# Optimization experiments

Hardware: AMD Instinct MI355X
Metric: run time of the kernel (lower is better)

## Reference

```python
import jax, jax.numpy as jnp
import numpy as np
from jax import lax

GAMMA_FLOW = 0.001
GAMMA_MASK = 0.0005
INTERP_RATIOS = (0.5,)


def setup_inputs() -> dict:
    key = jax.random.key(0)
    k1, k2, k3 = jax.random.split(key, 3)
    N, H, W, Ce = 8, 512, 512, 32
    frames = jax.random.uniform(k1, (N, H, W, 6), dtype=jnp.float32)
    encoded = jax.random.normal(k2, (N, H, W, Ce), dtype=jnp.float32)
    # small init so tanh is not saturated, like a trained conv head
    conv_w = jax.random.normal(k3, (3, 3, Ce, 3), dtype=jnp.float32) * 0.05
    conv_b = jnp.zeros((3,), dtype=jnp.float32)
    return {"frames": frames, "encoded": encoded, "conv_w": conv_w, "conv_b": conv_b}


def _total_variation(x):
    # matches tf.image.total_variation summed over the batch
    return (jnp.sum(jnp.abs(x[:, 1:] - x[:, :-1])) +
            jnp.sum(jnp.abs(x[:, :, 1:] - x[:, :, :-1])))


def _bilinear_interp(image, new_hh, new_ww):
    # image: [N,H,W,C]; new_hh/new_ww: [N,H,W] normalized coords in [-1,1]
    N, H, W, C = image.shape
    hh = (new_hh + 1.0) * (H - 1) / 2.0
    ww = (new_ww + 1.0) * (W - 1) / 2.0
    h0 = jnp.floor(hh).astype(jnp.int32)
    w0 = jnp.floor(ww).astype(jnp.int32)
    h1 = jnp.clip(h0 + 1, 0, H - 1)
    w1 = jnp.clip(w0 + 1, 0, W - 1)
    h0 = jnp.clip(h0, 0, H - 1)
    w0 = jnp.clip(w0, 0, W - 1)
    img_flat = image.reshape(N, H * W, C)

    def gather(h, w):
        idx = (h * W + w).reshape(N, H * W, 1)
        return jnp.take_along_axis(img_flat, idx, axis=1).reshape(N, H, W, C)

    ru = gather(h0, w0)
    rd = gather(h1, w0)
    lu = gather(h0, w1)
    ld = gather(h1, w1)
    h1f = h1.astype(hh.dtype)
    w1f = w1.astype(ww.dtype)
    w_ru = ((h1f - hh) * (w1f - ww))[..., None]
    w_rd = ((1.0 - (h1f - hh)) * (w1f - ww))[..., None]
    w_lu = ((h1f - hh) * (1.0 - (w1f - ww)))[..., None]
    w_ld = ((1.0 - (h1f - hh)) * (1.0 - (w1f - ww)))[..., None]
    return w_ru * ru + w_rd * rd + w_lu * lu + w_ld * ld


def reference(frames, encoded, conv_w, conv_b):
    frame0 = frames[..., 0:3]
    frame1 = frames[..., 3:6]
    N, H, W, _ = frame0.shape
    # 3x3 SAME conv + tanh (the layer's float32 conv head)
    net = jnp.tanh(
        lax.conv_general_dilated(encoded, conv_w, (1, 1), 'SAME',
                                 dimension_numbers=('NHWC', 'HWIO', 'NHWC'))
        + conv_b)
    flow = net[..., 0:2]

    hh = jnp.broadcast_to(jnp.linspace(-1.0, 1.0, H)[None, :, None], (N, H, W))
    ww = jnp.broadcast_to(jnp.linspace(-1.0, 1.0, W)[None, None, :], (N, H, W))

    total_pixels = float(N * H * W * 3)
    tv_loss = GAMMA_FLOW * _total_variation(flow) / total_pixels

    output_frames = []
    for i, alpha in enumerate(INTERP_RATIOS):
        mask = net[..., i + 2:i + 3]
        tv_loss = tv_loss + GAMMA_MASK * _total_variation(mask) / total_pixels
        coor_h_0 = hh + flow[..., 0] * alpha
        coor_w_0 = ww + flow[..., 1] * alpha
        coor_h_1 = hh - flow[..., 0] * (1.0 - alpha)
        coor_w_1 = ww - flow[..., 1] * (1.0 - alpha)
        out0 = _bilinear_interp(frame0, coor_h_0, coor_w_0)
        out1 = _bilinear_interp(frame1, coor_h_1, coor_w_1)
        m = 0.5 * (1.0 + mask)
        output_frames.append(m * out0 + (1.0 - m) * out1)
    stacked = jnp.concatenate(output_frames, axis=-1)
    return stacked, flow, tv_loss
```

## Files before the change

kernel.cpp:

```cpp
#include <hip/hip_runtime.h>
#include <hip/hip_fp16.h>
#include <math.h>

#define HH 512
#define WW 512
#define NIMG 8
#define NPIX (NIMG * HH * WW)
#define GAMMA_FLOW 0.001f
#define GAMMA_MASK 0.0005f
#define INV_TOTAL (1.0f / (float)(NPIX * 3))

#define CVT_BLOCKS  (NPIX / 256)
#define CONV_BLOCKS (NPIX / 128)
#define FAT_BLOCKS  (CVT_BLOCKS + CONV_BLOCKS)

__device__ __forceinline__ float tanh_fast(float x)
{
    float e = __expf(2.0f * x);
    return 1.0f - 2.0f / (e + 1.0f);
}

__device__ __forceinline__ void fma12(float acc[3], const float wf[12],
                                      float4 x)
{
    float xv[4] = {x.x, x.y, x.z, x.w};
#pragma unroll
    for (int k = 0; k < 4; ++k) {
        acc[0] = fmaf(xv[k], wf[k * 3 + 0], acc[0]);
        acc[1] = fmaf(xv[k], wf[k * 3 + 1], acc[1]);
        acc[2] = fmaf(xv[k], wf[k * 3 + 2], acc[2]);
    }
}

__global__ __launch_bounds__(256, 4) void fat_kernel(
    const float* __restrict__ enc, const float* __restrict__ cw,
    const float* __restrict__ cb, const float* __restrict__ frames,
    float* __restrict__ flow, float* __restrict__ mask,
    __half* __restrict__ f0h, __half* __restrict__ f1h,
    float* __restrict__ tv_out)
{
    int bid = blockIdx.x;

    if (bid % 3 == 0) {
        int ci = bid / 3;
        int t  = ci * 256 + threadIdx.x;
        if (t == 0) tv_out[0] = 0.0f;
        const float2* fp = reinterpret_cast<const float2*>(frames + (size_t)t * 6);
        float2 v0 = fp[0], v1 = fp[1], v2 = fp[2];
        __half2 a = __floats2half2_rn(v0.x, v0.y);
        __half2 b = __floats2half2_rn(v1.x, 0.0f);
        __half2 c = __floats2half2_rn(v1.y, v2.x);
        __half2 d = __floats2half2_rn(v2.y, 0.0f);
        __half2* p0 = reinterpret_cast<__half2*>(f0h) + (size_t)t * 2;
        __half2* p1 = reinterpret_cast<__half2*>(f1h) + (size_t)t * 2;
        p0[0] = a; p0[1] = b;
        p1[0] = c; p1[1] = d;
        return;
    }

    int ci  = bid - (bid + 2) / 3;
    int wb  = (ci & 7) * (CONV_BLOCKS / 8) + (ci >> 3);
    int px0 = wb * 128;
    int n = px0 >> 18;
    int h = (px0 >> 9) & (HH - 1);

    int tid  = threadIdx.x;
    int wv   = tid >> 6;
    int lane = tid & 63;
    int pg   = lane >> 3;
    int c4   = lane & 7;

    int wbase = (px0 & (WW - 1)) + wv * 32;
    int pxb   = wbase + pg * 4;

    const float4* cwB = reinterpret_cast<const float4*>(cw) + c4 * 3;
    const float* imgbase = enc + ((size_t)n * HH) * (WW * 32);

    float acc[4][3];
#pragma unroll
    for (int p = 0; p < 4; ++p)
        acc[p][0] = acc[p][1] = acc[p][2] = 0.0f;

    bool edge = (wbase == 0) || (wbase == WW - 32);

#pragma unroll
    for (int kh = 0; kh < 3; ++kh) {
        int hr = h + kh - 1;
        if ((unsigned)hr >= (unsigned)HH) continue;
        const float* rowp = imgbase + (size_t)hr * (WW * 32);

        float4 win[6];
        if (!edge) {
            const float* pB = rowp + (pxb - 1) * 32 + c4 * 4;
#pragma unroll
            for (int j = 0; j < 6; ++j)
                win[j] = *reinterpret_cast<const float4*>(pB + j * 32);
        } else {
#pragma unroll
            for (int j = 0; j < 6; ++j) {
                int col = pxb + j - 1;
                win[j] = make_float4(0.f, 0.f, 0.f, 0.f);
                if ((unsigned)col < (unsigned)WW)
                    win[j] = *reinterpret_cast<const float4*>(
                                 rowp + (size_t)col * 32 + c4 * 4);
            }
        }

#pragma unroll
        for (int kw = 0; kw < 3; ++kw) {
            int t = kh * 3 + kw;
            float wf[12];
            *reinterpret_cast<float4*>(&wf[0]) = cwB[t * 24 + 0];
            *reinterpret_cast<float4*>(&wf[4]) = cwB[t * 24 + 1];
            *reinterpret_cast<float4*>(&wf[8]) = cwB[t * 24 + 2];
#pragma unroll
            for (int p = 0; p < 4; ++p)
                fma12(acc[p], wf, win[p + kw]);
        }
    }

    float b0 = cb[0], b1 = cb[1], b2 = cb[2];
    size_t rowidx = ((size_t)n * HH + h) * WW;

#pragma unroll
    for (int p = 0; p < 4; ++p) {
#pragma unroll
        for (int off = 1; off < 8; off <<= 1) {
            acc[p][0] += __shfl_xor(acc[p][0], off);
            acc[p][1] += __shfl_xor(acc[p][1], off);
            acc[p][2] += __shfl_xor(acc[p][2], off);
        }
    }
    if (c4 == 0) {
#pragma unroll
        for (int p = 0; p < 4; ++p) {
            size_t idx = rowidx + (size_t)(pxb + p);
            *reinterpret_cast<float2*>(flow + idx * 2) =
                make_float2(tanh_fast(acc[p][0] + b0),
                            tanh_fast(acc[p][1] + b1));
            mask[idx] = tanh_fast(acc[p][2] + b2);
        }
    }
}

__device__ __forceinline__ void bilerp_h(const __half* __restrict__ img,
                                         float ch, float cwv, float out[3])
{
    float hp = (ch + 1.0f) * 255.5f;
    float wp = (cwv + 1.0f) * 255.5f;
    int h0 = (int)floorf(hp);
    int w0 = (int)floorf(wp);
    int h1  = min(max(h0 + 1, 0), HH - 1);
    int w1  = min(max(w0 + 1, 0), WW - 1);
    int h0c = min(max(h0, 0), HH - 1);
    int w0c = min(max(w0, 0), WW - 1);
    float wh = (float)h1 - hp;
    float wv = (float)w1 - wp;
    float w_ru = wh * wv;
    float w_rd = (1.0f - wh) * wv;
    float w_lu = wh * (1.0f - wv);
    float w_ld = (1.0f - wh) * (1.0f - wv);

    int q = min(w0c, WW - 2);
    bool Ahi = (w0c != q);
    bool Bhi = (w1 == q + 1);
    float4 U = *reinterpret_cast<const float4*>(img + (size_t)(((h0c << 9) + q) << 2));
    float4 D = *reinterpret_cast<const float4*>(img + (size_t)(((h1  << 9) + q) << 2));
    float ru_ab = Ahi ? U.z : U.x, ru_c = Ahi ? U.w : U.y;
    float rd_ab = Ahi ? D.z : D.x, rd_c = Ahi ? D.w : D.y;
    float lu_ab = Bhi ? U.z : U.x, lu_c = Bhi ? U.w : U.y;
    float ld_ab = Bhi ? D.z : D.x, ld_c = Bhi ? D.w : D.y;

    float2 ruA = __half22float2(*reinterpret_cast<__half2*>(&ru_ab));
    float2 rdA = __half22float2(*reinterpret_cast<__half2*>(&rd_ab));
    float2 luA = __half22float2(*reinterpret_cast<__half2*>(&lu_ab));
    float2 ldA = __half22float2(*reinterpret_cast<__half2*>(&ld_ab));
    float ruZ = __half2float(reinterpret_cast<__half2*>(&ru_c)->x);
    float rdZ = __half2float(reinterpret_cast<__half2*>(&rd_c)->x);
    float luZ = __half2float(reinterpret_cast<__half2*>(&lu_c)->x);
    float ldZ = __half2float(reinterpret_cast<__half2*>(&ld_c)->x);

    out[0] = w_ru * ruA.x + w_rd * rdA.x + w_lu * luA.x + w_ld * ldA.x;
    out[1] = w_ru * ruA.y + w_rd * rdA.y + w_lu * luA.y + w_ld * ldA.y;
    out[2] = w_ru * ruZ   + w_rd * rdZ   + w_lu * luZ   + w_ld * ldZ;
}

__global__ __launch_bounds__(256, 4) void interp_tv_kernel(
    const __half* __restrict__ f0h, const __half* __restrict__ f1h,
    const float* __restrict__ flow, const float* __restrict__ mask,
    float* __restrict__ stacked, float* __restrict__ tv_out)
{
    int bid = blockIdx.x;
    int wb  = (bid & 7) * (NPIX / 2048 / 8) + (bid >> 3);
    int idx0 = wb * 2048 + (int)threadIdx.x * 8;
    int w0 = idx0 & (WW - 1);
    int h  = (idx0 >> 9) & (HH - 1);
    int n  = idx0 >> 18;

    float4 fl[4];
#pragma unroll
    for (int j = 0; j < 4; ++j)
        fl[j] = *reinterpret_cast<const float4*>(flow + (size_t)idx0 * 2 + j * 4);
    float4 mkA = *reinterpret_cast<const float4*>(mask + idx0);
    float4 mkB = *reinterpret_cast<const float4*>(mask + idx0 + 4);
    const float* flp = reinterpret_cast<const float*>(fl);
    float mkp[8] = {mkA.x, mkA.y, mkA.z, mkA.w, mkB.x, mkB.y, mkB.z, mkB.w};

    float hhv = -1.0f + (float)h * (2.0f / 511.0f);

    const __half* i0 = f0h + (size_t)n * (HH * WW * 4);
    const __half* i1 = f1h + (size_t)n * (HH * WW * 4);

    float res[24];
#pragma unroll
    for (int p = 0; p < 8; ++p) {
        float wvx = -1.0f + (float)(w0 + p) * (2.0f / 511.0f);
        float fx = flp[p * 2], fy = flp[p * 2 + 1];
        float o0[3], o1[3];
        bilerp_h(i0, hhv + fx * 0.5f, wvx + fy * 0.5f, o0);
        bilerp_h(i1, hhv - fx * 0.5f, wvx - fy * 0.5f, o1);
        float m = 0.5f * (1.0f + mkp[p]), om = 1.0f - m;
#pragma unroll
        for (int c = 0; c < 3; ++c)
            res[p * 3 + c] = m * o0[c] + om * o1[c];
    }
    float4* sp = reinterpret_cast<float4*>(stacked + (size_t)idx0 * 3);
#pragma unroll
    for (int j = 0; j < 6; ++j)
        sp[j] = make_float4(res[j * 4], res[j * 4 + 1],
                            res[j * 4 + 2], res[j * 4 + 3]);

    float tvf = 0.0f, tvm = 0.0f;
#pragma unroll
    for (int p = 0; p < 7; ++p) {
        tvf += fabsf(flp[p * 2 + 2] - flp[p * 2])
             + fabsf(flp[p * 2 + 3] - flp[p * 2 + 1]);
        tvm += fabsf(mkp[p + 1] - mkp[p]);
    }
    if (w0 < WW - 8) {
        float2 flr = *reinterpret_cast<const float2*>(flow + (size_t)(idx0 + 8) * 2);
        float  mkr = mask[idx0 + 8];
        tvf += fabsf(flr.x - flp[14]) + fabsf(flr.y - flp[15]);
        tvm += fabsf(mkr - mkp[7]);
    }
    if (h < HH - 1) {
#pragma unroll
        for (int j = 0; j < 4; ++j) {
            float4 fd = *reinterpret_cast<const float4*>(
                            flow + (size_t)(idx0 + WW) * 2 + j * 4);
            tvf += fabsf(fd.x - flp[j * 4 + 0]) + fabsf(fd.y - flp[j * 4 + 1])
                 + fabsf(fd.z - flp[j * 4 + 2]) + fabsf(fd.w - flp[j * 4 + 3]);
        }
        float4 mdA = *reinterpret_cast<const float4*>(mask + idx0 + WW);
        float4 mdB = *reinterpret_cast<const float4*>(mask + idx0 + WW + 4);
        tvm += fabsf(mdA.x - mkp[0]) + fabsf(mdA.y - mkp[1])
             + fabsf(mdA.z - mkp[2]) + fabsf(mdA.w - mkp[3])
             + fabsf(mdB.x - mkp[4]) + fabsf(mdB.y - mkp[5])
             + fabsf(mdB.z - mkp[6]) + fabsf(mdB.w - mkp[7]);
    }
    float tv = GAMMA_FLOW * tvf + GAMMA_MASK * tvm;
#pragma unroll
    for (int off = 32; off > 0; off >>= 1) tv += __shfl_xor(tv, off);
    if ((threadIdx.x & 63) == 0) atomicAdd(tv_out, tv * INV_TOTAL);
}

extern "C" void kernel_launch(void* const* d_in, const int* in_sizes, int n_in,
                              void* d_out, int out_size, void* d_ws, size_t ws_size,
                              hipStream_t stream)
{
    const float* frames  = (const float*)d_in[0];
    const float* encoded = (const float*)d_in[1];
    const float* conv_w  = (const float*)d_in[2];
    const float* conv_b  = (const float*)d_in[3];

    float* out     = (float*)d_out;
    float* stacked = out;
    float* flow    = out + (size_t)NPIX * 3;
    float* tv      = out + (size_t)NPIX * 5;

    const size_t frame_bytes = (size_t)NPIX * 4 * sizeof(__half);
    __half* f0h = (__half*)d_ws;
    __half* f1h = (__half*)((char*)d_ws + frame_bytes);
    float*  mask = (float*)((char*)d_ws + 2 * frame_bytes);

    fat_kernel<<<FAT_BLOCKS, 256, 0, stream>>>(
        encoded, conv_w, conv_b, frames, flow, mask, f0h, f1h, tv);
    interp_tv_kernel<<<NPIX / 2048, 256, 0, stream>>>(
        f0h, f1h, flow, mask, stacked, tv);
}
```

Baseline: 223.6 us.

## Split conv: half in fused cvt kernel, half in 8-pixel-per-thread conv kernel

The fused kernel now computes the conv for only the first half of the pixels, interleaved one-to-one with the frame-conversion blocks. A new conv8_kernel handles the second half, with each thread computing 8 output pixels from a 10-column sliding window. This is meant to reuse loaded encoder data across more outputs and to write flow and mask with wider vector stores. In exchange it adds a third launch and higher register pressure (launch bounds lowered to 2).

New measurement: 273.3 us. 1.22x slower.

```diff
diff --git a/kernel.cpp b/kernel.cpp
--- a/kernel.cpp
+++ b/kernel.cpp
@@ -10,9 +10,11 @@
 #define GAMMA_MASK 0.0005f
 #define INV_TOTAL (1.0f / (float)(NPIX * 3))
 
-#define CVT_BLOCKS  (NPIX / 256)
-#define CONV_BLOCKS (NPIX / 128)
-#define FAT_BLOCKS  (CVT_BLOCKS + CONV_BLOCKS)
+#define HALF_PIX     (NPIX / 2)
+#define CVT_BLOCKS   (NPIX / 256)
+#define CONVA_BLOCKS (HALF_PIX / 128)
+#define FAT_BLOCKS   (CVT_BLOCKS + CONVA_BLOCKS)
+#define CONV8_BLOCKS (HALF_PIX / 256)
 
 __device__ __forceinline__ float tanh_fast(float x)
 {
@@ -41,8 +43,8 @@
 {
     int bid = blockIdx.x;
 
-    if (bid % 3 == 0) {
-        int ci = bid / 3;
+    if ((bid & 1) == 0) {
+        int ci = bid >> 1;
         int t  = ci * 256 + threadIdx.x;
         if (t == 0) tv_out[0] = 0.0f;
         const float2* fp = reinterpret_cast<const float2*>(frames + (size_t)t * 6);
@@ -58,8 +60,8 @@
         return;
     }
 
-    int ci  = bid - (bid + 2) / 3;
-    int wb  = (ci & 7) * (CONV_BLOCKS / 8) + (ci >> 3);
+    int ci  = bid >> 1;
+    int wb  = (ci & 7) * (CONVA_BLOCKS / 8) + (ci >> 3);
     int px0 = wb * 128;
     int n = px0 >> 18;
     int h = (px0 >> 9) & (HH - 1);
@@ -140,6 +142,103 @@
                             tanh_fast(acc[p][1] + b1));
             mask[idx] = tanh_fast(acc[p][2] + b2);
         }
+    }
+}
+
+__global__ __launch_bounds__(256, 2) void conv8_kernel(
+    const float* __restrict__ enc, const float* __restrict__ cw,
+    const float* __restrict__ cb, float* __restrict__ flow,
+    float* __restrict__ mask)
+{
+    int bid = blockIdx.x;
+    int wb  = (bid & 7) * (CONV8_BLOCKS / 8) + (bid >> 3);
+    int px0 = HALF_PIX + wb * 256;
+    int n = px0 >> 18;
+    int h = (px0 >> 9) & (HH - 1);
+
+    int tid  = threadIdx.x;
+    int wv   = tid >> 6;
+    int lane = tid & 63;
+    int pg   = lane >> 3;
+    int c4   = lane & 7;
+
+    int wbase = (px0 & (WW - 1)) + wv * 64;
+    int pxb   = wbase + pg * 8;
+
+    const float4* cwB = reinterpret_cast<const float4*>(cw) + c4 * 3;
+    const float* imgbase = enc + ((size_t)n * HH) * (WW * 32);
+
+    float acc[8][3];
+#pragma unroll
+    for (int p = 0; p < 8; ++p)
+        acc[p][0] = acc[p][1] = acc[p][2] = 0.0f;
+
+    bool edge = (wbase == 0) || (wbase == WW - 64);
+
+#pragma unroll
+    for (int kh = 0; kh < 3; ++kh) {
+        int hr = h + kh - 1;
+        if ((unsigned)hr >= (unsigned)HH) continue;
+        const float* rowp = imgbase + (size_t)hr * (WW * 32);
+
+        float4 win[10];
+        if (!edge) {
+            const float* pB = rowp + (pxb - 1) * 32 + c4 * 4;
+#pragma unroll
+            for (int j = 0; j < 10; ++j)
+                win[j] = *reinterpret_cast<const float4*>(pB + j * 32);
+        } else {
+#pragma unroll
+            for (int j = 0; j < 10; ++j) {
+                int col = pxb + j - 1;
+                win[j] = make_float4(0.f, 0.f, 0.f, 0.f);
+                if ((unsigned)col < (unsigned)WW)
+                    win[j] = *reinterpret_cast<const float4*>(
+                                 rowp + (size_t)col * 32 + c4 * 4);
+            }
+        }
+
+#pragma unroll
+        for (int kw = 0; kw < 3; ++kw) {
+            int t = kh * 3 + kw;
+            float wf[12];
+            *reinterpret_cast<float4*>(&wf[0]) = cwB[t * 24 + 0];
+            *reinterpret_cast<float4*>(&wf[4]) = cwB[t * 24 + 1];
+            *reinterpret_cast<float4*>(&wf[8]) = cwB[t * 24 + 2];
+#pragma unroll
+            for (int p = 0; p < 8; ++p)
+                fma12(acc[p], wf, win[p + kw]);
+        }
+    }
+
+    float b0 = cb[0], b1 = cb[1], b2 = cb[2];
+    size_t rowidx = ((size_t)n * HH + h) * WW;
+
+#pragma unroll
+    for (int p = 0; p < 8; ++p) {
+#pragma unroll
+        for (int off = 1; off < 8; off <<= 1) {
+            acc[p][0] += __shfl_xor(acc[p][0], off);
+            acc[p][1] += __shfl_xor(acc[p][1], off);
+            acc[p][2] += __shfl_xor(acc[p][2], off);
+        }
+    }
+    if (c4 == 0) {
+        float fl16[16], mk8[8];
+#pragma unroll
+        for (int p = 0; p < 8; ++p) {
+            fl16[p * 2 + 0] = tanh_fast(acc[p][0] + b0);
+            fl16[p * 2 + 1] = tanh_fast(acc[p][1] + b1);
+            mk8[p]          = tanh_fast(acc[p][2] + b2);
+        }
+        size_t idx = rowidx + (size_t)pxb;
+        float4* fp = reinterpret_cast<float4*>(flow + idx * 2);
+#pragma unroll
+        for (int j = 0; j < 4; ++j)
+            fp[j] = *reinterpret_cast<float4*>(&fl16[j * 4]);
+        float4* mp = reinterpret_cast<float4*>(mask + idx);
+        mp[0] = *reinterpret_cast<float4*>(&mk8[0]);
+        mp[1] = *reinterpret_cast<float4*>(&mk8[4]);
     }
 }
 
@@ -285,6 +384,8 @@
 
     fat_kernel<<<FAT_BLOCKS, 256, 0, stream>>>(
         encoded, conv_w, conv_b, frames, flow, mask, f0h, f1h, tv);
+    conv8_kernel<<<CONV8_BLOCKS, 256, 0, stream>>>(
+        encoded, conv_w, conv_b, flow, mask);
     interp_tv_kernel<<<NPIX / 2048, 256, 0, stream>>>(
         f0h, f1h, flow, mask, stacked, tv);
 }
```
